# Performance work log

Measured on AMD Instinct MI355X. Metric: run time of the kernel, lower is better.

Reference implementation:

```python
import jax, jax.numpy as jnp
import numpy as np

B, S, D_IN, D_HID, D_OUT, H = 2, 2048, 1024, 1024, 1024, 16
HD = D_HID // H  # head_dim = 64


def setup_inputs() -> dict:
    key = jax.random.key(0)
    ks = jax.random.split(key, 9)
    s_in = 1.0 / np.sqrt(D_IN)
    s_out = 1.0 / np.sqrt(D_OUT)
    return {
        "x": jax.random.normal(ks[0], (B, S, D_IN), dtype=jnp.float32),
        "Wq": jax.random.uniform(ks[1], (D_IN, D_HID), jnp.float32, -s_in, s_in),
        "bq": jax.random.uniform(ks[2], (D_HID,), jnp.float32, -s_in, s_in),
        "Wk": jax.random.uniform(ks[3], (D_IN, D_HID), jnp.float32, -s_in, s_in),
        "bk": jax.random.uniform(ks[4], (D_HID,), jnp.float32, -s_in, s_in),
        "Wv": jax.random.uniform(ks[5], (D_IN, D_OUT), jnp.float32, -s_in, s_in),
        "bv": jax.random.uniform(ks[6], (D_OUT,), jnp.float32, -s_in, s_in),
        "Wo": jax.random.uniform(ks[7], (D_OUT, D_OUT), jnp.float32, -s_out, s_out),
        "bo": jax.random.uniform(ks[8], (D_OUT,), jnp.float32, -s_out, s_out),
    }


def reference(x, Wq, bq, Wk, bk, Wv, bv, Wo, bo):
    b, s, _ = x.shape
    q = (x @ Wq + bq).reshape(b, s, H, HD)  # [B,S,H,HD]
    k = (x @ Wk + bk).reshape(b, s, H, HD)
    v = (x @ Wv + bv).reshape(b, s, H, HD)
    scores = jnp.einsum("bqhd,bkhd->bhqk", q, k) / jnp.sqrt(jnp.float32(HD))
    attn = jax.nn.softmax(scores, axis=-1)  # [B,H,S,S]
    ctx = jnp.einsum("bhqk,bkhd->bqhd", attn, v).reshape(b, s, D_HID)
    return ctx @ Wo + bo
```

## Files before the change

### kernel.cpp

```cpp
#include <hip/hip_runtime.h>
#include <stdint.h>

typedef __attribute__((ext_vector_type(8))) short short8v;
typedef __attribute__((ext_vector_type(4))) short short4v;
typedef __attribute__((ext_vector_type(4))) float float4v;
typedef __attribute__((ext_vector_type(4))) unsigned short ushort4v;
typedef __attribute__((ext_vector_type(4))) float floatvec4;
typedef __attribute__((ext_vector_type(2))) unsigned int uint2v;
typedef __attribute__((ext_vector_type(4))) unsigned int uint4v;
typedef __attribute__((ext_vector_type(8))) unsigned short ushort8v;

#define DEVI __device__ __forceinline__

DEVI unsigned short f2bf(float f) {
    unsigned int u = __builtin_bit_cast(unsigned int, f);
    u += 0x7FFFu + ((u >> 16) & 1u);
    return (unsigned short)(u >> 16);
}

DEVI unsigned int pk2bf(float a, float b) {
#if defined(__has_builtin) && __has_builtin(__builtin_amdgcn_cvt_pk_bf16_f32)
    auto r = __builtin_amdgcn_cvt_pk_bf16_f32(a, b);
    unsigned int u;
    __builtin_memcpy(&u, &r, 4);
    return u;
#else
    return (unsigned int)f2bf(a) | ((unsigned int)f2bf(b) << 16);
#endif
}

DEVI float ex2(float x) {
#if defined(__has_builtin) && __has_builtin(__builtin_amdgcn_exp2f)
    return __builtin_amdgcn_exp2f(x);
#else
    return __builtin_exp2f(x);
#endif
}

DEVI uint2v pl32swap(unsigned int d, unsigned int s) {
#if defined(__has_builtin) && __has_builtin(__builtin_amdgcn_permlane32_swap)
    return __builtin_amdgcn_permlane32_swap(d, s, false, false);
#else
    const int hi = (int)(threadIdx.x & 32);
    unsigned int dp = __shfl_xor(d, 32), sp = __shfl_xor(s, 32);
    return (uint2v){hi ? sp : d, hi ? s : dp};
#endif
}
DEVI uint2v pl16swap(unsigned int d, unsigned int s) {
#if defined(__has_builtin) && __has_builtin(__builtin_amdgcn_permlane16_swap)
    return __builtin_amdgcn_permlane16_swap(d, s, false, false);
#else
    const int lo = (int)(threadIdx.x & 16);
    unsigned int dp = __shfl_xor(d, 16), sp = __shfl_xor(s, 16);
    return (uint2v){lo ? sp : d, lo ? s : dp};
#endif
}

typedef __attribute__((address_space(1))) void GV;
typedef __attribute__((address_space(3))) void LV;
DEVI void gl2lds16(const void* g, void* l) {
    __builtin_amdgcn_global_load_lds((GV*)g, (LV*)l, 16, 0, 0);
}

__global__ void prep_kernel(const float* __restrict__ x, unsigned short* __restrict__ xb,
                            const float* __restrict__ W0, const float* __restrict__ W1,
                            const float* __restrict__ W2, const float* __restrict__ W3,
                            unsigned short* __restrict__ D0, unsigned short* __restrict__ D1,
                            unsigned short* __restrict__ D2, unsigned short* __restrict__ D3) {
    const int bid = blockIdx.x, tid = threadIdx.x;
    if (bid < 4096) {
        const int i = (bid * 256 + tid) * 4;
        const floatvec4 v = *(const floatvec4*)&x[i];
        ushort4v o;
#pragma unroll
        for (int r = 0; r < 4; r++) o[r] = f2bf(v[r]);
        *(ushort4v*)&xb[i] = o;
        return;
    }
    __shared__ float t[32][33];
    const int tcode = bid - 4096;
    const int z = tcode >> 10, rem = tcode & 1023;
    const int by = rem >> 5, bx = rem & 31;
    const int tx = tid & 31, ty = tid >> 5;
    const float* W = (z == 0) ? W0 : (z == 1) ? W1 : (z == 2) ? W2 : W3;
    unsigned short* D = (z == 0) ? D0 : (z == 1) ? D1 : (z == 2) ? D2 : D3;
#pragma unroll
    for (int i = 0; i < 4; i++)
        t[ty + i * 8][tx] = W[(size_t)(by * 32 + ty + i * 8) * 1024 + bx * 32 + tx];
    __syncthreads();
#pragma unroll
    for (int i = 0; i < 4; i++)
        D[(size_t)(bx * 32 + ty + i * 8) * 1024 + by * 32 + tx] = f2bf(t[tx][ty + i * 8]);
}

__global__ __launch_bounds__(256, 3) void qkv_gemm(
    const unsigned short* __restrict__ X, const unsigned short* __restrict__ Wt,
    const float* __restrict__ bq, const float* __restrict__ bk, const float* __restrict__ bv,
    unsigned short* __restrict__ qb, unsigned short* __restrict__ kb,
    unsigned short* __restrict__ vtb)
{
    __shared__ __align__(16) unsigned short As[128 * 64];
    __shared__ __align__(16) unsigned short Bs[128 * 64];
    const int tid = threadIdx.x, lane = tid & 63, wv = tid >> 6;
    const int quad = lane >> 4, l16 = lane & 15;
    const int w = blockIdx.x >> 3;
    const int n0 = (blockIdx.x & 7) * 128;
    const int row0 = blockIdx.y * 128;
    const unsigned short* Wsel = Wt + (size_t)w * (1024 * 1024);

    const int srow = lane >> 3;
    const int qsc = ((lane & 7) ^ (lane >> 3 & 7)) * 8;
    const int fsw = l16 & 7;
    const int wm = (wv >> 1) * 64, wn = (wv & 1) * 64;

    float4v acc[4][4];
#pragma unroll
    for (int i = 0; i < 4; i++)
#pragma unroll
        for (int j = 0; j < 4; j++) acc[i][j] = (float4v){0.f, 0.f, 0.f, 0.f};

    for (int k0 = 0; k0 < 1024; k0 += 64) {
        __syncthreads();
#pragma unroll
        for (int i = 0; i < 4; i++) {
            const int c = wv * 4 + i;
            gl2lds16(X + (size_t)(row0 + c * 8 + srow) * 1024 + k0 + qsc, As + c * 512);
            gl2lds16(Wsel + (size_t)(n0 + c * 8 + srow) * 1024 + k0 + qsc, Bs + c * 512);
        }
        __syncthreads();
#pragma unroll
        for (int kc = 0; kc < 2; kc++) {
            const int sl = (((kc * 4 + quad) ^ fsw) * 8);
            short8v a[4], b[4];
#pragma unroll
            for (int mt = 0; mt < 4; mt++)
                a[mt] = *(const short8v*)&As[(wm + mt * 16 + l16) * 64 + sl];
#pragma unroll
            for (int nt = 0; nt < 4; nt++)
                b[nt] = *(const short8v*)&Bs[(wn + nt * 16 + l16) * 64 + sl];
#pragma unroll
            for (int mt = 0; mt < 4; mt++)
#pragma unroll
                for (int nt = 0; nt < 4; nt++)
                    acc[mt][nt] = __builtin_amdgcn_mfma_f32_16x16x32_bf16(a[mt], b[nt], acc[mt][nt], 0, 0, 0);
        }
    }

    const float* bias = (w == 0) ? bq : (w == 1) ? bk : bv;
    const float scl = (w == 0) ? 0.18033688011112042f : 1.0f;
#pragma unroll
    for (int nt = 0; nt < 4; nt++) {
        const int col = n0 + wn + nt * 16 + l16;
        const float bb = bias[col];
        const int h = col >> 6, hd = col & 63;
#pragma unroll
        for (int mt = 0; mt < 4; mt++) {
            const int tok0 = row0 + wm + mt * 16 + quad * 4;
            const int b_ = tok0 >> 11, s0 = tok0 & 2047;
            if (w == 2) {
                ushort4v pk;
#pragma unroll
                for (int r = 0; r < 4; r++) pk[r] = f2bf(acc[mt][nt][r] + bb);
                *(ushort4v*)&vtb[(((size_t)b_ * 16 + h) * 64 + hd) * 2048 + s0] = pk;
            } else {
                unsigned short* dst = (w == 0) ? qb : kb;
#pragma unroll
                for (int r = 0; r < 4; r++)
                    dst[(((size_t)b_ * 16 + h) * 2048 + (s0 + r)) * 64 + hd] =
                        f2bf((acc[mt][nt][r] + bb) * scl);
            }
        }
    }
}

__global__ __launch_bounds__(256, 4) void attn_kernel(
    const unsigned short* __restrict__ qb, const unsigned short* __restrict__ kb,
    const unsigned short* __restrict__ vtb, unsigned short* __restrict__ ctxb)
{
    __shared__ __align__(16) unsigned short Kt[128 * 64];
    __shared__ __align__(16) unsigned short Vt[64 * 128];
    const int tid = threadIdx.x, lane = tid & 63, wv = tid >> 6;
    const int quad = lane >> 4, l16 = lane & 15;
    const int bh = blockIdx.x, qt = blockIdx.y;
    const size_t boff = (size_t)bh * (2048 * 64);
    const unsigned short* qp = qb + boff;
    const unsigned short* kp = kb + boff;
    const unsigned short* vp = vtb + boff;
    const int q0 = qt * 64 + wv * 16;

    short8v qf[2];
#pragma unroll
    for (int kc = 0; kc < 2; kc++)
        qf[kc] = *(const short8v*)&qp[(size_t)(q0 + l16) * 64 + kc * 32 + quad * 8];

    float4v accO[4];
#pragma unroll
    for (int ht = 0; ht < 4; ht++) accO[ht] = (float4v){0.f, 0.f, 0.f, 0.f};
    float4v accL = (float4v){0.f, 0.f, 0.f, 0.f};

    const ushort8v onesu = (ushort8v){0x3F80, 0x3F80, 0x3F80, 0x3F80,
                                      0x3F80, 0x3F80, 0x3F80, 0x3F80};
    const short8v ones = __builtin_bit_cast(short8v, onesu);

    const int krow = lane >> 3;
    const int kg = (lane & 7) ^ (lane >> 3);
    const int vrow = lane >> 4;
    const int rsw = l16 & 7;

    const int ktb0 = l16 * 64 + ((quad ^ rsw) * 8);
    const int ktb1 = l16 * 64 + (((4 + quad) ^ rsw) * 8);
    const int vrb = l16 * 128 + ((quad ^ (l16 & 3)) * 8);
    const int l12e = (l16 & 12) * 8;

    for (int kt0 = 0; kt0 < 2048; kt0 += 128) {
        __syncthreads();
#pragma unroll
        for (int i = 0; i < 4; i++) {
            const int c = wv * 4 + i;
            gl2lds16(kp + (size_t)(kt0 + c * 8 + krow) * 64 + kg * 8, Kt + c * 512);
            const int vr = c * 4 + vrow;
            const int vg = (lane & 15) ^ (vr & 15);
            gl2lds16(vp + (size_t)vr * 2048 + kt0 + vg * 8, Vt + c * 512);
        }
        __syncthreads();

        unsigned int pkr[8][2];
#pragma unroll
        for (int mt = 0; mt < 8; mt++) {
            const short8v a0 = *(const short8v*)&Kt[ktb0 + mt * 1024];
            const short8v a1 = *(const short8v*)&Kt[ktb1 + mt * 1024];
            float4v z = (float4v){0.f, 0.f, 0.f, 0.f};
            z = __builtin_amdgcn_mfma_f32_16x16x32_bf16(a0, qf[0], z, 0, 0, 0);
            z = __builtin_amdgcn_mfma_f32_16x16x32_bf16(a1, qf[1], z, 0, 0, 0);
            pkr[mt][0] = pk2bf(ex2(z[0]), ex2(z[1]));
            pkr[mt][1] = pk2bf(ex2(z[2]), ex2(z[3]));
        }

#pragma unroll
        for (int kc = 0; kc < 4; kc++) {
            const int roff = (kc * 32) ^ l12e;
            short8v bvv[4];
#pragma unroll
            for (int ht = 0; ht < 4; ht++)
                bvv[ht] = *(const short8v*)&Vt[vrb + roff + ht * 2048];
            const uint2v s0 = pl32swap(pkr[2 * kc][0], pkr[2 * kc + 1][0]);
            const uint2v s1 = pl32swap(pkr[2 * kc][1], pkr[2 * kc + 1][1]);
            const uint2v t0 = pl16swap(s0.x, s0.y);
            const uint2v t1 = pl16swap(s1.x, s1.y);
            const uint4v fu = (uint4v){t0.x, t1.x, t0.y, t1.y};
            const short8v ap = __builtin_bit_cast(short8v, fu);
            accL = __builtin_amdgcn_mfma_f32_16x16x32_bf16(ap, ones, accL, 0, 0, 0);
#pragma unroll
            for (int ht = 0; ht < 4; ht++)
                accO[ht] = __builtin_amdgcn_mfma_f32_16x16x32_bf16(ap, bvv[ht], accO[ht], 0, 0, 0);
        }
    }

    const int b_ = bh >> 4, h = bh & 15;
#pragma unroll
    for (int r = 0; r < 4; r++) {
        const int s = q0 + quad * 4 + r;
        const float inv = 1.0f / accL[r];
#pragma unroll
        for (int ht = 0; ht < 4; ht++) {
            const int hd = ht * 16 + l16;
            ctxb[((size_t)(b_ * 2048 + s)) * 1024 + h * 64 + hd] = f2bf(accO[ht][r] * inv);
        }
    }
}

__global__ __launch_bounds__(256, 2) void out_gemm(
    const unsigned short* __restrict__ ctx, const unsigned short* __restrict__ Wot,
    const float* __restrict__ bo, float* __restrict__ out)
{
    __shared__ __align__(16) unsigned short As[128 * 64];
    __shared__ __align__(16) unsigned short Bs[64 * 64];
    const int tid = threadIdx.x, lane = tid & 63, wv = tid >> 6;
    const int quad = lane >> 4, l16 = lane & 15;
    const int n0 = blockIdx.x * 64;
    const int row0 = blockIdx.y * 128;

    const int srow = lane >> 3;
    const int qsc = ((lane & 7) ^ (lane >> 3 & 7)) * 8;
    const int fsw = l16 & 7;
    const int wm = (wv & 1) * 64, wn = (wv >> 1) * 32;

    float4v acc[4][2];
#pragma unroll
    for (int i = 0; i < 4; i++)
#pragma unroll
        for (int j = 0; j < 2; j++) acc[i][j] = (float4v){0.f, 0.f, 0.f, 0.f};

    for (int k0 = 0; k0 < 1024; k0 += 64) {
        __syncthreads();
#pragma unroll
        for (int i = 0; i < 6; i++) {
            const int c = wv * 6 + i;
            if (c < 16)
                gl2lds16(ctx + (size_t)(row0 + c * 8 + srow) * 1024 + k0 + qsc, As + c * 512);
            else
                gl2lds16(Wot + (size_t)(n0 + (c - 16) * 8 + srow) * 1024 + k0 + qsc,
                         Bs + (c - 16) * 512);
        }
        __syncthreads();
#pragma unroll
        for (int kc = 0; kc < 2; kc++) {
            const int sl = (((kc * 4 + quad) ^ fsw) * 8);
            short8v a[4], b[2];
#pragma unroll
            for (int mt = 0; mt < 4; mt++)
                a[mt] = *(const short8v*)&As[(wm + mt * 16 + l16) * 64 + sl];
#pragma unroll
            for (int nt = 0; nt < 2; nt++)
                b[nt] = *(const short8v*)&Bs[(wn + nt * 16 + l16) * 64 + sl];
#pragma unroll
            for (int mt = 0; mt < 4; mt++)
#pragma unroll
                for (int nt = 0; nt < 2; nt++)
                    acc[mt][nt] = __builtin_amdgcn_mfma_f32_16x16x32_bf16(a[mt], b[nt], acc[mt][nt], 0, 0, 0);
        }
    }

#pragma unroll
    for (int nt = 0; nt < 2; nt++) {
        const int col = n0 + wn + nt * 16 + l16;
        const float bb = bo[col];
#pragma unroll
        for (int mt = 0; mt < 4; mt++) {
            const int tok0 = row0 + wm + mt * 16 + quad * 4;
#pragma unroll
            for (int r = 0; r < 4; r++)
                out[(size_t)(tok0 + r) * 1024 + col] = acc[mt][nt][r] + bb;
        }
    }
}

extern "C" void kernel_launch(void* const* d_in, const int* in_sizes, int n_in,
                              void* d_out, int out_size, void* d_ws, size_t ws_size,
                              hipStream_t stream) {
    const float* x  = (const float*)d_in[0];
    const float* Wq = (const float*)d_in[1];
    const float* bq = (const float*)d_in[2];
    const float* Wk = (const float*)d_in[3];
    const float* bk = (const float*)d_in[4];
    const float* Wv = (const float*)d_in[5];
    const float* bv = (const float*)d_in[6];
    const float* Wo = (const float*)d_in[7];
    const float* bo = (const float*)d_in[8];
    float* out = (float*)d_out;

    char* ws = (char*)d_ws;
    unsigned short* xb   = (unsigned short*)(ws);
    unsigned short* qbuf = (unsigned short*)(ws + (8u << 20));
    unsigned short* kbuf = (unsigned short*)(ws + (16u << 20));
    unsigned short* vtb  = (unsigned short*)(ws + (24u << 20));
    unsigned short* wt   = (unsigned short*)(ws + (32u << 20));
    unsigned short* wot  = (unsigned short*)(ws + (38u << 20));

    prep_kernel<<<8192, 256, 0, stream>>>(x, xb, Wq, Wk, Wv, Wo,
                                          wt, wt + (1u << 20), wt + (2u << 20), wot);
    qkv_gemm<<<dim3(24, 32), 256, 0, stream>>>(xb, wt, bq, bk, bv, qbuf, kbuf, vtb);
    attn_kernel<<<dim3(32, 32), 256, 0, stream>>>(qbuf, kbuf, vtb, xb );
    out_gemm<<<dim3(16, 32), 256, 0, stream>>>(xb, wot, bo, out);
}
```

Measured before the change: 187.4 us.

## Split attention over two KV halves with partial sums and combine kernel

The attention kernel now splits the key/value sequence into two halves along a new grid z dimension. Each block writes unnormalized fp32 partial outputs and row sums, and a new combine kernel adds them, normalizes and writes bf16 context. The KV tile shrinks from 128 to 64 keys to cut shared memory, and occupancy is raised to 8 blocks, doubling the block count to fill more CUs. The cost is extra fp32 partial traffic (one buffer aliased onto the output buffer), an extra launch, and the split only runs if the workspace is large enough. Softmax has no max subtraction, so summing the partials is exact.

```diff
diff --git a/kernel.cpp b/kernel.cpp
--- a/kernel.cpp
+++ b/kernel.cpp
@@ -173,15 +173,24 @@
     }
 }
 
-__global__ __launch_bounds__(256, 4) void attn_kernel(
+__global__ __launch_bounds__(256, 8) void attn_kernel(
     const unsigned short* __restrict__ qb, const unsigned short* __restrict__ kb,
-    const unsigned short* __restrict__ vtb, unsigned short* __restrict__ ctxb)
+    const unsigned short* __restrict__ vtb, unsigned short* __restrict__ ctxb,
+    float* __restrict__ pO0, float* __restrict__ pO1,
+    float* __restrict__ pL0, float* __restrict__ pL1)
 {
-    __shared__ __align__(16) unsigned short Kt[128 * 64];
-    __shared__ __align__(16) unsigned short Vt[64 * 128];
+    __shared__ __align__(16) unsigned short Kt[64 * 64];
+    __shared__ __align__(16) unsigned short Vt[64 * 64];
     const int tid = threadIdx.x, lane = tid & 63, wv = tid >> 6;
     const int quad = lane >> 4, l16 = lane & 15;
     const int bh = blockIdx.x, qt = blockIdx.y;
+    const int half = blockIdx.z;
+    const bool partial = (gridDim.z == 2);
+    const int kv0 = half << 10;
+    const int kvend = partial ? (kv0 + 1024) : 2048;
+    float* __restrict__ pO = half ? pO1 : pO0;
+    float* __restrict__ pL = half ? pL1 : pL0;
+
     const size_t boff = (size_t)bh * (2048 * 64);
     const unsigned short* qp = qb + boff;
     const unsigned short* kp = kb + boff;
@@ -202,33 +211,28 @@
                                       0x3F80, 0x3F80, 0x3F80, 0x3F80};
     const short8v ones = __builtin_bit_cast(short8v, onesu);
 
-    const int krow = lane >> 3;
-    const int kg = (lane & 7) ^ (lane >> 3);
-    const int vrow = lane >> 4;
+    const int srow8 = lane >> 3;
+    const int sg = ((lane & 7) ^ srow8) * 8;
     const int rsw = l16 & 7;
 
-    const int ktb0 = l16 * 64 + ((quad ^ rsw) * 8);
-    const int ktb1 = l16 * 64 + (((4 + quad) ^ rsw) * 8);
-    const int vrb = l16 * 128 + ((quad ^ (l16 & 3)) * 8);
-    const int l12e = (l16 & 12) * 8;
-
-    for (int kt0 = 0; kt0 < 2048; kt0 += 128) {
-        __syncthreads();
-#pragma unroll
-        for (int i = 0; i < 4; i++) {
-            const int c = wv * 4 + i;
-            gl2lds16(kp + (size_t)(kt0 + c * 8 + krow) * 64 + kg * 8, Kt + c * 512);
-            const int vr = c * 4 + vrow;
-            const int vg = (lane & 15) ^ (vr & 15);
-            gl2lds16(vp + (size_t)vr * 2048 + kt0 + vg * 8, Vt + c * 512);
-        }
-        __syncthreads();
-
-        unsigned int pkr[8][2];
-#pragma unroll
-        for (int mt = 0; mt < 8; mt++) {
-            const short8v a0 = *(const short8v*)&Kt[ktb0 + mt * 1024];
-            const short8v a1 = *(const short8v*)&Kt[ktb1 + mt * 1024];
+    const int fb0 = l16 * 64 + ((quad ^ rsw) * 8);
+    const int fb1 = l16 * 64 + (((4 + quad) ^ rsw) * 8);
+
+    for (int kt = kv0; kt < kvend; kt += 64) {
+        __syncthreads();
+#pragma unroll
+        for (int i = 0; i < 2; i++) {
+            const int c = wv * 2 + i;
+            gl2lds16(kp + (size_t)(kt + c * 8 + srow8) * 64 + sg, Kt + c * 512);
+            gl2lds16(vp + (size_t)(c * 8 + srow8) * 2048 + kt + sg, Vt + c * 512);
+        }
+        __syncthreads();
+
+        unsigned int pkr[4][2];
+#pragma unroll
+        for (int mt = 0; mt < 4; mt++) {
+            const short8v a0 = *(const short8v*)&Kt[fb0 + mt * 1024];
+            const short8v a1 = *(const short8v*)&Kt[fb1 + mt * 1024];
             float4v z = (float4v){0.f, 0.f, 0.f, 0.f};
             z = __builtin_amdgcn_mfma_f32_16x16x32_bf16(a0, qf[0], z, 0, 0, 0);
             z = __builtin_amdgcn_mfma_f32_16x16x32_bf16(a1, qf[1], z, 0, 0, 0);
@@ -237,12 +241,7 @@
         }
 
 #pragma unroll
-        for (int kc = 0; kc < 4; kc++) {
-            const int roff = (kc * 32) ^ l12e;
-            short8v bvv[4];
-#pragma unroll
-            for (int ht = 0; ht < 4; ht++)
-                bvv[ht] = *(const short8v*)&Vt[vrb + roff + ht * 2048];
+        for (int kc = 0; kc < 2; kc++) {
             const uint2v s0 = pl32swap(pkr[2 * kc][0], pkr[2 * kc + 1][0]);
             const uint2v s1 = pl32swap(pkr[2 * kc][1], pkr[2 * kc + 1][1]);
             const uint2v t0 = pl16swap(s0.x, s0.y);
@@ -250,23 +249,58 @@
             const uint4v fu = (uint4v){t0.x, t1.x, t0.y, t1.y};
             const short8v ap = __builtin_bit_cast(short8v, fu);
             accL = __builtin_amdgcn_mfma_f32_16x16x32_bf16(ap, ones, accL, 0, 0, 0);
-#pragma unroll
-            for (int ht = 0; ht < 4; ht++)
-                accO[ht] = __builtin_amdgcn_mfma_f32_16x16x32_bf16(ap, bvv[ht], accO[ht], 0, 0, 0);
+            const int vb = kc ? fb1 : fb0;
+#pragma unroll
+            for (int ht = 0; ht < 4; ht++) {
+                const short8v bv = *(const short8v*)&Vt[vb + ht * 1024];
+                accO[ht] = __builtin_amdgcn_mfma_f32_16x16x32_bf16(ap, bv, accO[ht], 0, 0, 0);
+            }
         }
     }
 
     const int b_ = bh >> 4, h = bh & 15;
-#pragma unroll
-    for (int r = 0; r < 4; r++) {
-        const int s = q0 + quad * 4 + r;
-        const float inv = 1.0f / accL[r];
-#pragma unroll
-        for (int ht = 0; ht < 4; ht++) {
-            const int hd = ht * 16 + l16;
-            ctxb[((size_t)(b_ * 2048 + s)) * 1024 + h * 64 + hd] = f2bf(accO[ht][r] * inv);
-        }
-    }
+    if (partial) {
+#pragma unroll
+        for (int r = 0; r < 4; r++) {
+            const int s = q0 + quad * 4 + r;
+            float* dst = pO + ((size_t)(b_ * 2048 + s)) * 1024 + h * 64;
+#pragma unroll
+            for (int ht = 0; ht < 4; ht++) dst[ht * 16 + l16] = accO[ht][r];
+        }
+        if (l16 == 0) {
+#pragma unroll
+            for (int r = 0; r < 4; r++)
+                pL[((size_t)b_ * 16 + h) * 2048 + q0 + quad * 4 + r] = accL[r];
+        }
+    } else {
+#pragma unroll
+        for (int r = 0; r < 4; r++) {
+            const int s = q0 + quad * 4 + r;
+            const float inv = 1.0f / accL[r];
+#pragma unroll
+            for (int ht = 0; ht < 4; ht++) {
+                const int hd = ht * 16 + l16;
+                ctxb[((size_t)(b_ * 2048 + s)) * 1024 + h * 64 + hd] = f2bf(accO[ht][r] * inv);
+            }
+        }
+    }
+}
+
+__global__ __launch_bounds__(256) void combine_kernel(
+    const float* __restrict__ pO0, const float* __restrict__ pO1,
+    const float* __restrict__ pL0, const float* __restrict__ pL1,
+    unsigned short* __restrict__ ctxb)
+{
+    const int i4 = (blockIdx.x * 256 + threadIdx.x) * 4;
+    const int h = (i4 >> 6) & 15, s = (i4 >> 10) & 2047, b_ = i4 >> 21;
+    const int li = (b_ * 16 + h) * 2048 + s;
+    const float inv = 1.0f / (pL0[li] + pL1[li]);
+    const floatvec4 o0 = *(const floatvec4*)&pO0[i4];
+    const floatvec4 o1 = *(const floatvec4*)&pO1[i4];
+    ushort4v o;
+#pragma unroll
+    for (int j = 0; j < 4; j++) o[j] = f2bf((o0[j] + o1[j]) * inv);
+    *(ushort4v*)&ctxb[i4] = o;
 }
 
 __global__ __launch_bounds__(256, 2) void out_gemm(
@@ -356,10 +390,23 @@
     unsigned short* vtb  = (unsigned short*)(ws + (24u << 20));
     unsigned short* wt   = (unsigned short*)(ws + (32u << 20));
     unsigned short* wot  = (unsigned short*)(ws + (38u << 20));
+    float* pO0 = (float*)out;
+    float* pO1 = (float*)(ws + (40u << 20));
+    float* pL0 = (float*)(ws + (56u << 20));
+    float* pL1 = pL0 + 65536;
+
+    const bool split = ws_size >= ((size_t)57 << 20);
 
     prep_kernel<<<8192, 256, 0, stream>>>(x, xb, Wq, Wk, Wv, Wo,
                                           wt, wt + (1u << 20), wt + (2u << 20), wot);
     qkv_gemm<<<dim3(24, 32), 256, 0, stream>>>(xb, wt, bq, bk, bv, qbuf, kbuf, vtb);
-    attn_kernel<<<dim3(32, 32), 256, 0, stream>>>(qbuf, kbuf, vtb, xb );
+    if (split) {
+        attn_kernel<<<dim3(32, 32, 2), 256, 0, stream>>>(qbuf, kbuf, vtb, xb,
+                                                         pO0, pO1, pL0, pL1);
+        combine_kernel<<<4096, 256, 0, stream>>>(pO0, pO1, pL0, pL1, xb );
+    } else {
+        attn_kernel<<<dim3(32, 32, 1), 256, 0, stream>>>(qbuf, kbuf, vtb, xb ,
+                                                         nullptr, nullptr, nullptr, nullptr);
+    }
     out_gemm<<<dim3(16, 32), 256, 0, stream>>>(xb, wot, bo, out);
 }
```

Measured after the change: 205.3 us. 9.6% more time.
